# Optimization experiments

Hardware: AMD Instinct MI355X
Metric: run time of the kernel (lower is better)

## Reference

```python
import jax, jax.numpy as jnp
import numpy as np

K = 3       # strip kernel taps
G = 2       # groups
PAD = (K - 1) // 2  # dilation=1


def setup_inputs() -> dict:
    key = jax.random.key(0)
    k1, k2, k3, k4, k5 = jax.random.split(key, 5)
    n, c, h, w = 8, 96, 256, 256
    x = jax.random.normal(k1, (n, c, h, w), dtype=jnp.float32)
    Wconv = jax.random.normal(k2, (G * K, c), dtype=jnp.float32) * 0.1   # 1x1 conv weight
    inside_all = jax.random.normal(k3, (c, 1, 1), dtype=jnp.float32) * 0.1
    lamb_l = jax.random.normal(k4, (c,), dtype=jnp.float32) * 0.1
    lamb_h = jax.random.normal(k5, (c,), dtype=jnp.float32) * 0.1
    return {"x": x, "Wconv": Wconv, "inside_all": inside_all,
            "lamb_l": lamb_l, "lamb_h": lamb_h}


def reference(x, Wconv, inside_all, lamb_l, lamb_h):
    n, c, h, w = x.shape
    cg = c // G
    # dynamic per-(sample, group) filter from global average pool + 1x1 conv + tanh
    m = x.mean(axis=(2, 3))                       # (n, c)
    filt = jnp.tanh(m @ Wconv.T).reshape(n, G, K)  # (n, G, K)
    # reflection pad along width (H=True -> horizontal strip)
    xp = jnp.pad(x, ((0, 0), (0, 0), (0, 0), (PAD, PAD)), mode="reflect")
    xr = xp.reshape(n, G, cg, h, w + 2 * PAD)
    # sliding-window multiply-accumulate over K taps (no unfold materialization)
    out = xr[..., 0:w] * filt[:, :, None, None, None, 0]
    for i in range(1, K):
        out = out + xr[..., i:i + w] * filt[:, :, None, None, None, i]
    out = out.reshape(n, c, h, w)
    # gated low/high residual mix; gap averages over width for H=True
    gap = x.mean(axis=3, keepdims=True)            # (n, c, h, 1)
    out_low = (out * (inside_all + 1.0) - inside_all * gap) * lamb_l[None, :, None, None]
    out_high = x * (lamb_h[None, :, None, None] + 1.0)
    return out_low + out_high
```

## Files before the change

kernel.cpp:

```cpp
#include <hip/hip_runtime.h>
#include <math.h>

#define NN 8
#define CC 96
#define HH 256
#define WW 256
#define GG 2
#define KK 3
#define CPG (CC / GG)
#define HWD (HH * WW)
#define CHUNKS 8

typedef float fvec4 __attribute__((ext_vector_type(4)));

__global__ __launch_bounds__(256) void partial_kernel(
    const float* __restrict__ x, float* __restrict__ mp) {
    const int b = blockIdx.x;
    const int nc = b >> 3;
    const int chunk = b & 7;
    const int t = threadIdx.x;
    const fvec4* xp = (const fvec4*)x + (size_t)nc * (HWD / 4)
                      + (size_t)chunk * (HWD / 4 / CHUNKS);
    float s = 0.f;
#pragma unroll
    for (int i = 0; i < HWD / 4 / CHUNKS / 256; ++i) {
        fvec4 v = xp[i * 256 + t];
        s += (v.x + v.y) + (v.z + v.w);
    }
#pragma unroll
    for (int off = 32; off; off >>= 1) s += __shfl_down(s, off, 64);
    __shared__ float ls[4];
    if ((t & 63) == 0) ls[t >> 6] = s;
    __syncthreads();
    if (t == 0) mp[b] = (ls[0] + ls[1]) + (ls[2] + ls[3]);
}

__global__ __launch_bounds__(256) void main_kernel(
    const float* __restrict__ x, const float* __restrict__ mp,
    const float* __restrict__ Wconv, const float* __restrict__ inside_all,
    const float* __restrict__ lamb_l, const float* __restrict__ lamb_h,
    float* __restrict__ out) {
    const int bb = blockIdx.x;
    const int nc = bb >> 4;
    const int rblk = bb & 15;
    const int t = threadIdx.x;
    const int wave = t >> 6;
    const int lane = t & 63;
    const int c = nc % CC;
    const int n = nc / CC;
    const int g = c / CPG;

    __shared__ float msh[CC];
    __shared__ float fsh[KK];
    if (t < CC) {
        const float* pr = mp + ((size_t)n * CC + t) * CHUNKS;
        float a0 = 0.f;
#pragma unroll
        for (int k = 0; k < CHUNKS; ++k) a0 += pr[k];
        msh[t] = a0;
    }
    __syncthreads();
    if (t < KK) {
        const float* Wr = Wconv + (g * KK + t) * CC;
        float acc = 0.f;
#pragma unroll
        for (int j = 0; j < CC; ++j) acc += msh[j] * Wr[j];
        fsh[t] = tanhf(acc * (1.0f / (float)HWD));
    }
    __syncthreads();
    const float f0 = fsh[0], f1 = fsh[1], f2 = fsh[2];
    const float ia = inside_all[c];
    const float ll = lamb_l[c];
    const float lh1 = lamb_h[c] + 1.0f;
    const float a = ia + 1.0f;

    const int row0 = (rblk << 4) + (wave << 2);
    const size_t base = ((size_t)nc * HH + row0) * WW;
    fvec4 v0 = __builtin_nontemporal_load((const fvec4*)(x + base + 0 * WW) + lane);
    fvec4 v1 = __builtin_nontemporal_load((const fvec4*)(x + base + 1 * WW) + lane);
    fvec4 v2 = __builtin_nontemporal_load((const fvec4*)(x + base + 2 * WW) + lane);
    fvec4 v3 = __builtin_nontemporal_load((const fvec4*)(x + base + 3 * WW) + lane);

    float s0 = (v0.x + v0.y) + (v0.z + v0.w);
    float s1 = (v1.x + v1.y) + (v1.z + v1.w);
    float s2 = (v2.x + v2.y) + (v2.z + v2.w);
    float s3 = (v3.x + v3.y) + (v3.z + v3.w);
#pragma unroll
    for (int off = 1; off < 64; off <<= 1) {
        s0 += __shfl_xor(s0, off, 64);
        s1 += __shfl_xor(s1, off, 64);
        s2 += __shfl_xor(s2, off, 64);
        s3 += __shfl_xor(s3, off, 64);
    }

#pragma unroll
    for (int r = 0; r < 4; ++r) {
        const fvec4 v = (r == 0) ? v0 : (r == 1) ? v1 : (r == 2) ? v2 : v3;
        const float rs = (r == 0) ? s0 : (r == 1) ? s1 : (r == 2) ? s2 : s3;
        const float gap = rs * (1.0f / (float)WW);

        const float left = __shfl_up(v.w, 1, 64);
        const float right = __shfl_down(v.x, 1, 64);
        const float xm1 = (lane == 0) ? v.y : left;
        const float xp1 = (lane == 63) ? v.z : right;

        const float c0 = f0 * xm1 + f1 * v.x + f2 * v.y;
        const float c1 = f0 * v.x + f1 * v.y + f2 * v.z;
        const float c2 = f0 * v.y + f1 * v.z + f2 * v.w;
        const float c3 = f0 * v.z + f1 * v.w + f2 * xp1;

        const float bterm = ia * gap;
        fvec4 o;
        o.x = (c0 * a - bterm) * ll + v.x * lh1;
        o.y = (c1 * a - bterm) * ll + v.y * lh1;
        o.z = (c2 * a - bterm) * ll + v.z * lh1;
        o.w = (c3 * a - bterm) * ll + v.w * lh1;
        ((fvec4*)(out + base + r * WW))[lane] = o;
    }
}

extern "C" void kernel_launch(void* const* d_in, const int* in_sizes, int n_in,
                              void* d_out, int out_size, void* d_ws,
                              size_t ws_size, hipStream_t stream) {
    const float* x = (const float*)d_in[0];
    const float* Wconv = (const float*)d_in[1];
    const float* inside_all = (const float*)d_in[2];
    const float* lamb_l = (const float*)d_in[3];
    const float* lamb_h = (const float*)d_in[4];
    float* out = (float*)d_out;
    float* mp = (float*)d_ws;

    partial_kernel<<<NN * CC * CHUNKS, 256, 0, stream>>>(x, mp);
    main_kernel<<<NN * CC * (HH / 16), 256, 0, stream>>>(
        x, mp, Wconv, inside_all, lamb_l, lamb_h, out);
}
```

Before: 111.0 us.

## Interleave per-sample reduction and main kernels so x is reread from cache

Splits the two-pass work into per-sample launches. Each sample's partial-sum kernel is followed by the previous sample's main kernel, so the second read of each roughly 25 MB slice of x can hit in the last-level cache instead of going back to HBM. The main kernel now uses regular loads for x so the data stays cached, and nontemporal stores for the output so the output does not evict it. The cost is sixteen kernel launches instead of two, with smaller grids and possible launch gaps or tail effects.

```diff
diff --git a/kernel.cpp b/kernel.cpp
--- a/kernel.cpp
+++ b/kernel.cpp
@@ -10,16 +10,17 @@
 #define CPG (CC / GG)
 #define HWD (HH * WW)
 #define CHUNKS 8
+#define SLICE_F (CC * HWD)
 
 typedef float fvec4 __attribute__((ext_vector_type(4)));
 
-__global__ __launch_bounds__(256) void partial_kernel(
-    const float* __restrict__ x, float* __restrict__ mp) {
+__global__ __launch_bounds__(256) void partial_kernel_s(
+    const float* __restrict__ x_n, float* __restrict__ mp_n) {
     const int b = blockIdx.x;
-    const int nc = b >> 3;
+    const int cl = b >> 3;
     const int chunk = b & 7;
     const int t = threadIdx.x;
-    const fvec4* xp = (const fvec4*)x + (size_t)nc * (HWD / 4)
+    const fvec4* xp = (const fvec4*)x_n + (size_t)cl * (HWD / 4)
                       + (size_t)chunk * (HWD / 4 / CHUNKS);
     float s = 0.f;
 #pragma unroll
@@ -32,28 +33,26 @@
     __shared__ float ls[4];
     if ((t & 63) == 0) ls[t >> 6] = s;
     __syncthreads();
-    if (t == 0) mp[b] = (ls[0] + ls[1]) + (ls[2] + ls[3]);
+    if (t == 0) mp_n[b] = (ls[0] + ls[1]) + (ls[2] + ls[3]);
 }
 
-__global__ __launch_bounds__(256) void main_kernel(
-    const float* __restrict__ x, const float* __restrict__ mp,
+__global__ __launch_bounds__(256) void main_kernel_s(
+    const float* __restrict__ x_n, const float* __restrict__ mp_n,
     const float* __restrict__ Wconv, const float* __restrict__ inside_all,
     const float* __restrict__ lamb_l, const float* __restrict__ lamb_h,
-    float* __restrict__ out) {
+    float* __restrict__ out_n) {
     const int bb = blockIdx.x;
-    const int nc = bb >> 4;
+    const int c = bb >> 4;
     const int rblk = bb & 15;
     const int t = threadIdx.x;
     const int wave = t >> 6;
     const int lane = t & 63;
-    const int c = nc % CC;
-    const int n = nc / CC;
     const int g = c / CPG;
 
     __shared__ float msh[CC];
     __shared__ float fsh[KK];
     if (t < CC) {
-        const float* pr = mp + ((size_t)n * CC + t) * CHUNKS;
+        const float* pr = mp_n + (size_t)t * CHUNKS;
         float a0 = 0.f;
 #pragma unroll
         for (int k = 0; k < CHUNKS; ++k) a0 += pr[k];
@@ -75,11 +74,11 @@
     const float a = ia + 1.0f;
 
     const int row0 = (rblk << 4) + (wave << 2);
-    const size_t base = ((size_t)nc * HH + row0) * WW;
-    fvec4 v0 = __builtin_nontemporal_load((const fvec4*)(x + base + 0 * WW) + lane);
-    fvec4 v1 = __builtin_nontemporal_load((const fvec4*)(x + base + 1 * WW) + lane);
-    fvec4 v2 = __builtin_nontemporal_load((const fvec4*)(x + base + 2 * WW) + lane);
-    fvec4 v3 = __builtin_nontemporal_load((const fvec4*)(x + base + 3 * WW) + lane);
+    const size_t base = ((size_t)c * HH + row0) * WW;
+    fvec4 v0 = ((const fvec4*)(x_n + base + 0 * WW))[lane];
+    fvec4 v1 = ((const fvec4*)(x_n + base + 1 * WW))[lane];
+    fvec4 v2 = ((const fvec4*)(x_n + base + 2 * WW))[lane];
+    fvec4 v3 = ((const fvec4*)(x_n + base + 3 * WW))[lane];
 
     float s0 = (v0.x + v0.y) + (v0.z + v0.w);
     float s1 = (v1.x + v1.y) + (v1.z + v1.w);
@@ -115,7 +114,7 @@
         o.y = (c1 * a - bterm) * ll + v.y * lh1;
         o.z = (c2 * a - bterm) * ll + v.z * lh1;
         o.w = (c3 * a - bterm) * ll + v.w * lh1;
-        ((fvec4*)(out + base + r * WW))[lane] = o;
+        __builtin_nontemporal_store(o, (fvec4*)(out_n + base + r * WW) + lane);
     }
 }
 
@@ -130,7 +129,17 @@
     float* out = (float*)d_out;
     float* mp = (float*)d_ws;
 
-    partial_kernel<<<NN * CC * CHUNKS, 256, 0, stream>>>(x, mp);
-    main_kernel<<<NN * CC * (HH / 16), 256, 0, stream>>>(
-        x, mp, Wconv, inside_all, lamb_l, lamb_h, out);
+    for (int n = 0; n < NN; ++n) {
+        partial_kernel_s<<<CC * CHUNKS, 256, 0, stream>>>(
+            x + (size_t)n * SLICE_F, mp + (size_t)n * CC * CHUNKS);
+        if (n >= 1) {
+            const int p = n - 1;
+            main_kernel_s<<<CC * (HH / 16), 256, 0, stream>>>(
+                x + (size_t)p * SLICE_F, mp + (size_t)p * CC * CHUNKS, Wconv,
+                inside_all, lamb_l, lamb_h, out + (size_t)p * SLICE_F);
+        }
+    }
+    main_kernel_s<<<CC * (HH / 16), 256, 0, stream>>>(
+        x + (size_t)(NN - 1) * SLICE_F, mp + (size_t)(NN - 1) * CC * CHUNKS,
+        Wconv, inside_all, lamb_l, lamb_h, out + (size_t)(NN - 1) * SLICE_F);
 }
```

New measurement: 126.0 us. +13.5%, slower.
